# Kernel optimization log

Measured on AMD Instinct MI355X. Metric: run time of the kernel, lower is better.

## Reference

```python
import jax, jax.numpy as jnp
import numpy as np

N = 50000
E = 800000
D = 128  # in_channels == hidden_channels
NEG_SLOPE = 0.2


def setup_inputs() -> dict:
    key = jax.random.key(0)
    ks = jax.random.split(key, 20)
    x = jax.random.normal(ks[0], (N, D), dtype=jnp.float32)
    edge_index = jax.random.randint(ks[1], (2, E), 0, N, dtype=jnp.int64)
    inp = {"x": x, "edge_index": edge_index}
    # 3 GATv2 layers: lin_l (source), lin_r (target), att vector, bias. Glorot-ish scale.
    s = 1.0 / np.sqrt(D)
    for l in range(3):
        inp[f"Wl{l}"] = jax.random.normal(ks[2 + 4 * l], (D, D), dtype=jnp.float32) * s
        inp[f"Wr{l}"] = jax.random.normal(ks[3 + 4 * l], (D, D), dtype=jnp.float32) * s
        inp[f"att{l}"] = jax.random.normal(ks[4 + 4 * l], (D,), dtype=jnp.float32) * s
        inp[f"b{l}"] = jnp.zeros((D,), dtype=jnp.float32)
    return inp


def _gatv2_layer(x, src, dst, Wl, Wr, att, b):
    # PyG GATv2Conv, heads=1: xl = lin_l(x) (source side), xr = lin_r(x) (target side)
    xl = x @ Wl.T  # [N, D]
    xr = x @ Wr.T  # [N, D]
    m = xl[src] + xr[dst]                      # [E', D]
    m = jnp.where(m > 0, m, NEG_SLOPE * m)     # LeakyReLU(0.2)
    e = m @ att                                # [E'] attention logits
    # segment softmax over incoming edges of each dst node (numerically stable)
    emax = jnp.full((x.shape[0],), jnp.finfo(e.dtype).min, dtype=e.dtype).at[dst].max(e)
    ex = jnp.exp(e - emax[dst])
    denom = jnp.zeros((x.shape[0],), dtype=e.dtype).at[dst].add(ex)
    alpha = ex / denom[dst]                    # [E']
    out = jnp.zeros_like(xl).at[dst].add(alpha[:, None] * xl[src])
    return out + b


def reference(x, edge_index, Wl0, Wr0, att0, b0, Wl1, Wr1, att1, b1, Wl2, Wr2, att2, b2):
    n = x.shape[0]
    loops = jnp.arange(n, dtype=edge_index.dtype)
    src = jnp.concatenate([edge_index[0], loops])  # add_self_loops=True (PyG default)
    dst = jnp.concatenate([edge_index[1], loops])
    params = [(Wl0, Wr0, att0, b0), (Wl1, Wr1, att1, b1), (Wl2, Wr2, att2, b2)]
    h = x
    for (Wl, Wr, att, b) in params:
        h = _gatv2_layer(h, src, dst, Wl, Wr, att, b)
        h = jax.nn.gelu(h, approximate=False)  # F.gelu exact
        # dropout p=0.0 / eval mode -> identity
    return h
```

## Files before the change

kernel.cpp:

```cpp
#include <hip/hip_runtime.h>
#include <hip/hip_fp16.h>
#include <math.h>
#include <float.h>

#define NNODES 50000
#define NPAD   50048
#define NEDGES 800000
#define NETOT  (NEDGES + NNODES)
#define NBUCK  98
#define BCAP   12288
#define PCHUNK 2048

typedef __attribute__((ext_vector_type(8))) _Float16 hfrag;
typedef __attribute__((ext_vector_type(4))) float ffrag;
typedef __attribute__((ext_vector_type(8))) unsigned short ushort8;


__global__ __launch_bounds__(256) void convert_w(
    const float* __restrict__ w0, const float* __restrict__ w1,
    const float* __restrict__ w2, const float* __restrict__ w3,
    const float* __restrict__ w4, const float* __restrict__ w5,
    _Float16* __restrict__ bp)
{
  int g = blockIdx.x * 256 + threadIdx.x;
  int mat = g >> 11;
  int c = g & 2047;
  int tile_nl = c >> 8;
  int kb = (c >> 6) & 3;
  int lane = c & 63;
  int n_local = tile_nl * 16 + (lane & 15);
  int k0 = kb * 32 + (lane >> 4) * 8;
  const float* s = w0;
  if (mat == 1) s = w1; else if (mat == 2) s = w2; else if (mat == 3) s = w3;
  else if (mat == 4) s = w4; else if (mat == 5) s = w5;
  const float* src = s + n_local * 128 + k0;
  hfrag hv;
#pragma unroll
  for (int j = 0; j < 8; ++j) hv[j] = (_Float16)src[j];
  int layer = mat >> 1, half = mat & 1;
  int chunk = ((half * 8 + tile_nl) * 4 + kb) * 64 + lane;
  ((hfrag*)(bp + (size_t)layer * 32768))[chunk] = hv;
}

__global__ __launch_bounds__(256) void convert_x(
    const float* __restrict__ x, _Float16* __restrict__ ap)
{
  int g = blockIdx.x * 256 + threadIdx.x;
  if (g >= NNODES * 16) return;
  int tile_m = g >> 8;
  int kb = (g >> 6) & 3;
  int lane = g & 63;
  int m = tile_m * 16 + (lane & 15);
  int k0 = kb * 32 + (lane >> 4) * 8;
  const float4* src = (const float4*)(x + (size_t)m * 128 + k0);
  float4 v0 = src[0], v1 = src[1];
  hfrag hv;
  hv[0] = (_Float16)v0.x; hv[1] = (_Float16)v0.y;
  hv[2] = (_Float16)v0.z; hv[3] = (_Float16)v0.w;
  hv[4] = (_Float16)v1.x; hv[5] = (_Float16)v1.y;
  hv[6] = (_Float16)v1.z; hv[7] = (_Float16)v1.w;
  ((hfrag*)ap)[g] = hv;
}

__global__ __launch_bounds__(256) void partition_kernel(
    const int* __restrict__ ei, int* __restrict__ bcursor,
    unsigned* __restrict__ tmp)
{
  __shared__ unsigned stage[PCHUNK];
  __shared__ int cnt[128];
  __shared__ int lstart[NBUCK];
  __shared__ int gbase[NBUCK];
  __shared__ int lcur[NBUCK];
  const int t = threadIdx.x;
  const int e0 = blockIdx.x * PCHUNK;

  if (t < 128) cnt[t] = 0;
  __syncthreads();

  unsigned pk[8]; int pb[8]; int nv = 0;
#pragma unroll
  for (int i = 0; i < 8; ++i) {
    int e = e0 + t + i * 256;
    if (e < NETOT) {
      int s, d;
      if (e < NEDGES) { s = ei[e]; d = ei[NEDGES + e]; }
      else            { s = e - NEDGES; d = s; }
      int b = d >> 9;
      pk[nv] = (unsigned)s | ((unsigned)(d & 511) << 16) | ((unsigned)b << 25);
      pb[nv] = b;
      atomicAdd(&cnt[b], 1);
      ++nv;
    }
  }
  __syncthreads();

  int v = (t < 128) ? cnt[t] : 0;
  for (int off = 1; off < 128; off <<= 1) {
    int u = (t < 128 && t >= off) ? cnt[t - off] : 0;
    __syncthreads();
    if (t < 128) cnt[t] += u;
    __syncthreads();
  }
  if (t < NBUCK) {
    int excl = cnt[t] - v;
    lstart[t] = excl;
    lcur[t] = excl;
    gbase[t] = (v > 0) ? atomicAdd(&bcursor[t], v) : 0;
  }
  __syncthreads();

  for (int i = 0; i < nv; ++i) {
    int p = atomicAdd(&lcur[pb[i]], 1);
    stage[p] = pk[i];
  }
  __syncthreads();

  int total = cnt[NBUCK - 1];
  for (int j = t; j < total; j += 256) {
    unsigned w = stage[j];
    int b = (int)(w >> 25);
    int pos = gbase[b] + (j - lstart[b]);
    if (pos < BCAP) tmp[(size_t)b * BCAP + pos] = w;
  }
}

__global__ __launch_bounds__(256) void bucket_sort(
    const int* __restrict__ bcursor, const unsigned* __restrict__ tmp,
    int* __restrict__ rowptr, int* __restrict__ col)
{
  __shared__ int sh[512];
  __shared__ int cur[512];
  const int b = blockIdx.x;
  const int t = threadIdx.x;
  int nb = bcursor[b];
  if (nb > BCAP) nb = BCAP;

  int base = 0;
  for (int c = 0; c < b; ++c) base += bcursor[c];

  sh[t] = 0; sh[t + 256] = 0;
  __syncthreads();
  const unsigned* tb = tmp + (size_t)b * BCAP;
  for (int j = t; j < nb; j += 256)
    atomicAdd(&sh[(tb[j] >> 16) & 511], 1);
  __syncthreads();

  int c1 = sh[t], c2 = sh[t + 256];
  for (int off = 1; off < 512; off <<= 1) {
    int u1 = (t >= off) ? sh[t - off] : 0;
    int u2 = (t + 256 >= off) ? sh[t + 256 - off] : 0;
    __syncthreads();
    sh[t] += u1; sh[t + 256] += u2;
    __syncthreads();
  }
  int e1 = sh[t] - c1, e2 = sh[t + 256] - c2;
  cur[t] = e1; cur[t + 256] = e2;
  int g1 = b * 512 + t, g2 = b * 512 + t + 256;
  if (g1 < NNODES) rowptr[g1] = base + e1;
  if (g2 < NNODES) rowptr[g2] = base + e2;
  if (b == 0 && t == 0) rowptr[NNODES] = NETOT;
  __syncthreads();

  for (int j = t; j < nb; j += 256) {
    unsigned w = tb[j];
    int s = atomicAdd(&cur[(w >> 16) & 511], 1);
    col[base + s] = (int)(w & 0xFFFFu);
  }
}

__global__ __launch_bounds__(256) void gemm_mfma(
    const _Float16* __restrict__ ap, const _Float16* __restrict__ bp,
    ushort* __restrict__ xlh, float* __restrict__ xr)
{
  const int wave = threadIdx.x >> 6;
  const int lane = threadIdx.x & 63;
  const int l16  = lane & 15;
  const int kq   = lane >> 4;
  const int m0   = blockIdx.x * 32;
  const int tm0  = m0 >> 4;

  ffrag acc[2][4];
#pragma unroll
  for (int mt = 0; mt < 2; ++mt)
#pragma unroll
    for (int nt = 0; nt < 4; ++nt)
      acc[mt][nt] = (ffrag){0.f, 0.f, 0.f, 0.f};

#pragma unroll
  for (int kb = 0; kb < 4; ++kb) {
    hfrag ah[2], bh[4];
#pragma unroll
    for (int mt = 0; mt < 2; ++mt) {
      size_t o = (size_t)(((tm0 + mt) * 4 + kb) * 512 + lane * 8);
      ah[mt] = *(const hfrag*)&ap[o];
    }
#pragma unroll
    for (int nt = 0; nt < 4; ++nt) {
      size_t o = (size_t)((((wave * 4 + nt) * 4) + kb) * 512 + lane * 8);
      bh[nt] = *(const hfrag*)&bp[o];
    }
#pragma unroll
    for (int mt = 0; mt < 2; ++mt)
#pragma unroll
      for (int nt = 0; nt < 4; ++nt)
        acc[mt][nt] = __builtin_amdgcn_mfma_f32_16x16x32_f16(
            ah[mt], bh[nt], acc[mt][nt], 0, 0, 0);
  }

#pragma unroll
  for (int mt = 0; mt < 2; ++mt) {
    int mb = m0 + mt * 16 + kq * 4;
#pragma unroll
    for (int nt = 0; nt < 4; ++nt) {
      int ng = wave * 64 + nt * 16 + l16;
      if (ng < 128) {
#pragma unroll
        for (int r = 0; r < 4; ++r) {
          int m = mb + r;
          if (m < NNODES)
            ((__half*)xlh)[m * 128 + ng] = __float2half(acc[mt][nt][r]);
        }
      } else {
        int n = ng & 127;
#pragma unroll
        for (int r = 0; r < 4; ++r) {
          int m = mb + r;
          if (m < NNODES) xr[m * 128 + n] = acc[mt][nt][r];
        }
      }
    }
  }
}

static __device__ __forceinline__ void h8_to_f(
    const ushort8& v, float4& a, float4& b)
{
  a.x = __half2float(__ushort_as_half(v[0]));
  a.y = __half2float(__ushort_as_half(v[1]));
  a.z = __half2float(__ushort_as_half(v[2]));
  a.w = __half2float(__ushort_as_half(v[3]));
  b.x = __half2float(__ushort_as_half(v[4]));
  b.y = __half2float(__ushort_as_half(v[5]));
  b.z = __half2float(__ushort_as_half(v[6]));
  b.w = __half2float(__ushort_as_half(v[7]));
}

static __device__ __forceinline__ float edge_logit(
    const float4& a0, const float4& a1,
    const float4& xr0, const float4& xr1,
    const float4& t0, const float4& t1)
{
  float m, qa, qb;
  m = a0.x + xr0.x; m = fmaxf(m, 0.2f * m); qa = m * t0.x;
  m = a0.y + xr0.y; m = fmaxf(m, 0.2f * m); qa = fmaf(m, t0.y, qa);
  m = a0.z + xr0.z; m = fmaxf(m, 0.2f * m); qa = fmaf(m, t0.z, qa);
  m = a0.w + xr0.w; m = fmaxf(m, 0.2f * m); qa = fmaf(m, t0.w, qa);
  m = a1.x + xr1.x; m = fmaxf(m, 0.2f * m); qb = m * t1.x;
  m = a1.y + xr1.y; m = fmaxf(m, 0.2f * m); qb = fmaf(m, t1.y, qb);
  m = a1.z + xr1.z; m = fmaxf(m, 0.2f * m); qb = fmaf(m, t1.z, qb);
  m = a1.w + xr1.w; m = fmaxf(m, 0.2f * m); qb = fmaf(m, t1.w, qb);
  return qa + qb;
}

static __device__ __forceinline__ void facc(
    float4& a0, float4& a1, float w, const float4& v0, const float4& v1)
{
  a0.x = fmaf(w, v0.x, a0.x); a0.y = fmaf(w, v0.y, a0.y);
  a0.z = fmaf(w, v0.z, a0.z); a0.w = fmaf(w, v0.w, a0.w);
  a1.x = fmaf(w, v1.x, a1.x); a1.y = fmaf(w, v1.y, a1.y);
  a1.z = fmaf(w, v1.z, a1.z); a1.w = fmaf(w, v1.w, a1.w);
}

static __device__ __forceinline__ float gelu_exact(float v) {
  return 0.5f * v * (1.f + erff(v * 0.70710678118654752f));
}

__global__ __launch_bounds__(256) void agg_kernel(
    const int* __restrict__ rowptr, const int* __restrict__ col,
    const ushort* __restrict__ xlh, const float* __restrict__ xr,
    const float* __restrict__ att, const float* __restrict__ bias,
    float* __restrict__ hout, _Float16* __restrict__ ap, int last)
{
  const int tid = threadIdx.x;
  const int l16 = tid & 15;
  const int grp = tid >> 4;
  const int d   = blockIdx.x * 16 + grp;
  const int fb  = l16 * 2;

  const ushort8* xl8 = (const ushort8*)xlh;
  float4 xr0 = ((const float4*)xr)[d * 32 + fb];
  float4 xr1 = ((const float4*)xr)[d * 32 + fb + 1];
  float4 at0 = ((const float4*)att)[fb];
  float4 at1 = ((const float4*)att)[fb + 1];

  const int beg = rowptr[d], end = rowptr[d + 1];

  float dnE = 0.f, dnO = 0.f;
  float4 aE0 = {0,0,0,0}, aE1 = {0,0,0,0};
  float4 aO0 = {0,0,0,0}, aO1 = {0,0,0,0};

  for (int k = beg; k < end; k += 4) {
    const int  c0 = col[k];
    const bool v1 = (k + 1 < end);
    const bool v2 = (k + 2 < end);
    const bool v3 = (k + 3 < end);
    const int  c1 = col[v1 ? k + 1 : k];
    const int  c2 = col[v2 ? k + 2 : k];
    const int  c3 = col[v3 ? k + 3 : k];

    ushort8 Ar = xl8[c0 * 16 + l16];
    ushort8 Br = xl8[c1 * 16 + l16];
    ushort8 Cr = xl8[c2 * 16 + l16];
    ushort8 Dr = xl8[c3 * 16 + l16];

    float4 A0, A1, B0, B1, C0, C1, D0, D1;
    h8_to_f(Ar, A0, A1);
    h8_to_f(Br, B0, B1);
    h8_to_f(Cr, C0, C1);
    h8_to_f(Dr, D0, D1);

    float q0 = edge_logit(A0, A1, xr0, xr1, at0, at1);
    float q1 = edge_logit(B0, B1, xr0, xr1, at0, at1);
    float q2 = edge_logit(C0, C1, xr0, xr1, at0, at1);
    float q3 = edge_logit(D0, D1, xr0, xr1, at0, at1);
#pragma unroll
    for (int off = 8; off > 0; off >>= 1) {
      q0 += __shfl_xor(q0, off, 64);
      q1 += __shfl_xor(q1, off, 64);
      q2 += __shfl_xor(q2, off, 64);
      q3 += __shfl_xor(q3, off, 64);
    }
    float w0 = __expf(q0);
    float w1 = v1 ? __expf(q1) : 0.f;
    float w2 = v2 ? __expf(q2) : 0.f;
    float w3 = v3 ? __expf(q3) : 0.f;
    dnE += w0 + w2;
    dnO += w1 + w3;
    facc(aE0, aE1, w0, A0, A1);
    facc(aO0, aO1, w1, B0, B1);
    facc(aE0, aE1, w2, C0, C1);
    facc(aO0, aO1, w3, D0, D1);
  }

  const float dn = dnE + dnO;
  const float inv = 1.f / dn;
  float4 ac0, ac1;
  ac0.x = aE0.x + aO0.x; ac0.y = aE0.y + aO0.y;
  ac0.z = aE0.z + aO0.z; ac0.w = aE0.w + aO0.w;
  ac1.x = aE1.x + aO1.x; ac1.y = aE1.y + aO1.y;
  ac1.z = aE1.z + aO1.z; ac1.w = aE1.w + aO1.w;

  float4 bi0 = ((const float4*)bias)[fb];
  float4 bi1 = ((const float4*)bias)[fb + 1];
  float o0 = gelu_exact(fmaf(ac0.x, inv, bi0.x));
  float o1 = gelu_exact(fmaf(ac0.y, inv, bi0.y));
  float o2 = gelu_exact(fmaf(ac0.z, inv, bi0.z));
  float o3 = gelu_exact(fmaf(ac0.w, inv, bi0.w));
  float o4 = gelu_exact(fmaf(ac1.x, inv, bi1.x));
  float o5 = gelu_exact(fmaf(ac1.y, inv, bi1.y));
  float o6 = gelu_exact(fmaf(ac1.z, inv, bi1.z));
  float o7 = gelu_exact(fmaf(ac1.w, inv, bi1.w));

  if (last) {
    ((float4*)hout)[d * 32 + fb]     = make_float4(o0, o1, o2, o3);
    ((float4*)hout)[d * 32 + fb + 1] = make_float4(o4, o5, o6, o7);
  } else {
    hfrag hv;
    hv[0] = (_Float16)o0; hv[1] = (_Float16)o1;
    hv[2] = (_Float16)o2; hv[3] = (_Float16)o3;
    hv[4] = (_Float16)o4; hv[5] = (_Float16)o5;
    hv[6] = (_Float16)o6; hv[7] = (_Float16)o7;
    int chunk = ((d >> 4) * 4 + (l16 >> 2)) * 64 + (l16 & 3) * 16 + (d & 15);
    ((hfrag*)ap)[chunk] = hv;
  }
}

extern "C" void kernel_launch(void* const* d_in, const int* in_sizes, int n_in,
                              void* d_out, int out_size, void* d_ws, size_t ws_size,
                              hipStream_t stream)
{
  const float* x = (const float*)d_in[0];
  const int* ei = (const int*)d_in[1];
  const float *Wl[3], *Wr[3], *attv[3], *bv[3];
  for (int l = 0; l < 3; ++l) {
    Wl[l]   = (const float*)d_in[2 + 4 * l];
    Wr[l]   = (const float*)d_in[3 + 4 * l];
    attv[l] = (const float*)d_in[4 + 4 * l];
    bv[l]   = (const float*)d_in[5 + 4 * l];
  }

  char* base = (char*)d_ws;
  size_t off = 0;
  auto alloc = [&](size_t bytes) -> char* {
    char* p = base + off;
    off += (bytes + 255) & ~(size_t)255;
    return p;
  };
  _Float16* ap  = (_Float16*)alloc((size_t)NPAD * 128 * 2);
  _Float16* bp  = (_Float16*)alloc((size_t)3 * 256 * 128 * 2);
  ushort* xlh   = (ushort*)alloc((size_t)NNODES * 128 * 2);
  int* rowptr   = (int*)alloc((size_t)(NNODES + 1) * 4);
  int* col      = (int*)alloc((size_t)NETOT * 4);
  int* bcursor  = (int*)alloc((size_t)NBUCK * 4);
  unsigned* tmp = (unsigned*)alloc((size_t)NBUCK * BCAP * 4);
  float* xr     = (float*)d_out;
  (void)ws_size; (void)in_sizes; (void)n_in; (void)out_size;

  hipMemsetAsync(bcursor, 0, (size_t)NBUCK * 4, stream);
  convert_w<<<48, 256, 0, stream>>>(Wl[0], Wr[0], Wl[1], Wr[1], Wl[2], Wr[2],
                                    bp);
  convert_x<<<(NNODES * 16 + 255) / 256, 256, 0, stream>>>(x, ap);
  partition_kernel<<<(NETOT + PCHUNK - 1) / PCHUNK, 256, 0, stream>>>(
      ei, bcursor, tmp);
  bucket_sort<<<NBUCK, 256, 0, stream>>>(bcursor, tmp, rowptr, col);

  for (int l = 0; l < 3; ++l) {
    gemm_mfma<<<NPAD / 32, 256, 0, stream>>>(
        ap, bp + (size_t)l * 32768, xlh, xr);
    agg_kernel<<<NNODES / 16, 256, 0, stream>>>(
        rowptr, col, xlh, xr, attv[l], bv[l], (float*)d_out, ap,
        (l == 2) ? 1 : 0);
  }
}
```

Before: 318.4 us.

## Fuse prologue kernels, store xr in fp16, parallelize bucket base scan

Merges weight conversion, input conversion and edge partitioning into one prologue launch that branches on block index, removing two kernel launches. The target-side projection xr is now stored in fp16 in its own buffer instead of fp32 in the output buffer, halving its write and read traffic between the GEMM and aggregation kernels. The bucket sort computes its base offset with a shared-memory prefix scan instead of a serial loop per block. Storing xr in fp16 adds rounding error to the attention logits.

```diff
diff --git a/kernel.cpp b/kernel.cpp
--- a/kernel.cpp
+++ b/kernel.cpp
@@ -10,61 +10,23 @@
 #define NBUCK  98
 #define BCAP   12288
 #define PCHUNK 2048
+#define PBLK   416
+#define CWBLK  48
+#define CXBLK  3125
 
 typedef __attribute__((ext_vector_type(8))) _Float16 hfrag;
 typedef __attribute__((ext_vector_type(4))) float ffrag;
 typedef __attribute__((ext_vector_type(8))) unsigned short ushort8;
 
 
-__global__ __launch_bounds__(256) void convert_w(
+__global__ __launch_bounds__(256) void prologue_kernel(
+    const float* __restrict__ x,
     const float* __restrict__ w0, const float* __restrict__ w1,
     const float* __restrict__ w2, const float* __restrict__ w3,
     const float* __restrict__ w4, const float* __restrict__ w5,
-    _Float16* __restrict__ bp)
-{
-  int g = blockIdx.x * 256 + threadIdx.x;
-  int mat = g >> 11;
-  int c = g & 2047;
-  int tile_nl = c >> 8;
-  int kb = (c >> 6) & 3;
-  int lane = c & 63;
-  int n_local = tile_nl * 16 + (lane & 15);
-  int k0 = kb * 32 + (lane >> 4) * 8;
-  const float* s = w0;
-  if (mat == 1) s = w1; else if (mat == 2) s = w2; else if (mat == 3) s = w3;
-  else if (mat == 4) s = w4; else if (mat == 5) s = w5;
-  const float* src = s + n_local * 128 + k0;
-  hfrag hv;
-#pragma unroll
-  for (int j = 0; j < 8; ++j) hv[j] = (_Float16)src[j];
-  int layer = mat >> 1, half = mat & 1;
-  int chunk = ((half * 8 + tile_nl) * 4 + kb) * 64 + lane;
-  ((hfrag*)(bp + (size_t)layer * 32768))[chunk] = hv;
-}
-
-__global__ __launch_bounds__(256) void convert_x(
-    const float* __restrict__ x, _Float16* __restrict__ ap)
-{
-  int g = blockIdx.x * 256 + threadIdx.x;
-  if (g >= NNODES * 16) return;
-  int tile_m = g >> 8;
-  int kb = (g >> 6) & 3;
-  int lane = g & 63;
-  int m = tile_m * 16 + (lane & 15);
-  int k0 = kb * 32 + (lane >> 4) * 8;
-  const float4* src = (const float4*)(x + (size_t)m * 128 + k0);
-  float4 v0 = src[0], v1 = src[1];
-  hfrag hv;
-  hv[0] = (_Float16)v0.x; hv[1] = (_Float16)v0.y;
-  hv[2] = (_Float16)v0.z; hv[3] = (_Float16)v0.w;
-  hv[4] = (_Float16)v1.x; hv[5] = (_Float16)v1.y;
-  hv[6] = (_Float16)v1.z; hv[7] = (_Float16)v1.w;
-  ((hfrag*)ap)[g] = hv;
-}
-
-__global__ __launch_bounds__(256) void partition_kernel(
-    const int* __restrict__ ei, int* __restrict__ bcursor,
-    unsigned* __restrict__ tmp)
+    const int* __restrict__ ei,
+    _Float16* __restrict__ ap, _Float16* __restrict__ bp,
+    int* __restrict__ bcursor, unsigned* __restrict__ tmp)
 {
   __shared__ unsigned stage[PCHUNK];
   __shared__ int cnt[128];
@@ -72,55 +34,94 @@
   __shared__ int gbase[NBUCK];
   __shared__ int lcur[NBUCK];
   const int t = threadIdx.x;
-  const int e0 = blockIdx.x * PCHUNK;
-
-  if (t < 128) cnt[t] = 0;
-  __syncthreads();
-
-  unsigned pk[8]; int pb[8]; int nv = 0;
-#pragma unroll
-  for (int i = 0; i < 8; ++i) {
-    int e = e0 + t + i * 256;
-    if (e < NETOT) {
-      int s, d;
-      if (e < NEDGES) { s = ei[e]; d = ei[NEDGES + e]; }
-      else            { s = e - NEDGES; d = s; }
-      int b = d >> 9;
-      pk[nv] = (unsigned)s | ((unsigned)(d & 511) << 16) | ((unsigned)b << 25);
-      pb[nv] = b;
-      atomicAdd(&cnt[b], 1);
-      ++nv;
-    }
-  }
-  __syncthreads();
-
-  int v = (t < 128) ? cnt[t] : 0;
-  for (int off = 1; off < 128; off <<= 1) {
-    int u = (t < 128 && t >= off) ? cnt[t - off] : 0;
-    __syncthreads();
-    if (t < 128) cnt[t] += u;
-    __syncthreads();
-  }
-  if (t < NBUCK) {
-    int excl = cnt[t] - v;
-    lstart[t] = excl;
-    lcur[t] = excl;
-    gbase[t] = (v > 0) ? atomicAdd(&bcursor[t], v) : 0;
-  }
-  __syncthreads();
-
-  for (int i = 0; i < nv; ++i) {
-    int p = atomicAdd(&lcur[pb[i]], 1);
-    stage[p] = pk[i];
-  }
-  __syncthreads();
-
-  int total = cnt[NBUCK - 1];
-  for (int j = t; j < total; j += 256) {
-    unsigned w = stage[j];
-    int b = (int)(w >> 25);
-    int pos = gbase[b] + (j - lstart[b]);
-    if (pos < BCAP) tmp[(size_t)b * BCAP + pos] = w;
+  const int blk = blockIdx.x;
+
+  if (blk < PBLK) {
+    const int e0 = blk * PCHUNK;
+    if (t < 128) cnt[t] = 0;
+    __syncthreads();
+
+    unsigned pk[8]; int pb[8]; int nv = 0;
+#pragma unroll
+    for (int i = 0; i < 8; ++i) {
+      int e = e0 + t + i * 256;
+      if (e < NETOT) {
+        int s, d;
+        if (e < NEDGES) { s = ei[e]; d = ei[NEDGES + e]; }
+        else            { s = e - NEDGES; d = s; }
+        int b = d >> 9;
+        pk[nv] = (unsigned)s | ((unsigned)(d & 511) << 16) |
+                 ((unsigned)b << 25);
+        pb[nv] = b;
+        atomicAdd(&cnt[b], 1);
+        ++nv;
+      }
+    }
+    __syncthreads();
+
+    int v = (t < 128) ? cnt[t] : 0;
+    for (int off = 1; off < 128; off <<= 1) {
+      int u = (t < 128 && t >= off) ? cnt[t - off] : 0;
+      __syncthreads();
+      if (t < 128) cnt[t] += u;
+      __syncthreads();
+    }
+    if (t < NBUCK) {
+      int excl = cnt[t] - v;
+      lstart[t] = excl;
+      lcur[t] = excl;
+      gbase[t] = (v > 0) ? atomicAdd(&bcursor[t], v) : 0;
+    }
+    __syncthreads();
+
+    for (int i = 0; i < nv; ++i) {
+      int p = atomicAdd(&lcur[pb[i]], 1);
+      stage[p] = pk[i];
+    }
+    __syncthreads();
+
+    int total = cnt[NBUCK - 1];
+    for (int j = t; j < total; j += 256) {
+      unsigned w = stage[j];
+      int b = (int)(w >> 25);
+      int pos = gbase[b] + (j - lstart[b]);
+      if (pos < BCAP) tmp[(size_t)b * BCAP + pos] = w;
+    }
+  } else if (blk < PBLK + CWBLK) {
+    int g = (blk - PBLK) * 256 + t;
+    int mat = g >> 11;
+    int c = g & 2047;
+    int tile_nl = c >> 8;
+    int kb = (c >> 6) & 3;
+    int lane = c & 63;
+    int n_local = tile_nl * 16 + (lane & 15);
+    int k0 = kb * 32 + (lane >> 4) * 8;
+    const float* s = w0;
+    if (mat == 1) s = w1; else if (mat == 2) s = w2;
+    else if (mat == 3) s = w3; else if (mat == 4) s = w4;
+    else if (mat == 5) s = w5;
+    const float* src = s + n_local * 128 + k0;
+    hfrag hv;
+#pragma unroll
+    for (int j = 0; j < 8; ++j) hv[j] = (_Float16)src[j];
+    int layer = mat >> 1, half = mat & 1;
+    int chunk = ((half * 8 + tile_nl) * 4 + kb) * 64 + lane;
+    ((hfrag*)(bp + (size_t)layer * 32768))[chunk] = hv;
+  } else {
+    int g = (blk - PBLK - CWBLK) * 256 + t;
+    int tile_m = g >> 8;
+    int kb = (g >> 6) & 3;
+    int lane = g & 63;
+    int m = tile_m * 16 + (lane & 15);
+    int k0 = kb * 32 + (lane >> 4) * 8;
+    const float4* src = (const float4*)(x + (size_t)m * 128 + k0);
+    float4 v0 = src[0], v1 = src[1];
+    hfrag hv;
+    hv[0] = (_Float16)v0.x; hv[1] = (_Float16)v0.y;
+    hv[2] = (_Float16)v0.z; hv[3] = (_Float16)v0.w;
+    hv[4] = (_Float16)v1.x; hv[5] = (_Float16)v1.y;
+    hv[6] = (_Float16)v1.z; hv[7] = (_Float16)v1.w;
+    ((hfrag*)ap)[g] = hv;
   }
 }
 
@@ -132,11 +133,20 @@
   __shared__ int cur[512];
   const int b = blockIdx.x;
   const int t = threadIdx.x;
-  int nb = bcursor[b];
+
+  int bc = (t < NBUCK) ? bcursor[t] : 0;
+  if (t < 128) sh[t] = bc;
+  __syncthreads();
+  for (int off = 1; off < 128; off <<= 1) {
+    int u = (t < 128 && t >= off) ? sh[t - off] : 0;
+    __syncthreads();
+    if (t < 128) sh[t] += u;
+    __syncthreads();
+  }
+  const int base = (b > 0) ? sh[b - 1] : 0;
+  int nb = sh[b] - base;
   if (nb > BCAP) nb = BCAP;
-
-  int base = 0;
-  for (int c = 0; c < b; ++c) base += bcursor[c];
+  __syncthreads();
 
   sh[t] = 0; sh[t + 256] = 0;
   __syncthreads();
@@ -170,7 +180,7 @@
 
 __global__ __launch_bounds__(256) void gemm_mfma(
     const _Float16* __restrict__ ap, const _Float16* __restrict__ bp,
-    ushort* __restrict__ xlh, float* __restrict__ xr)
+    _Float16* __restrict__ xlh, _Float16* __restrict__ xrh)
 {
   const int wave = threadIdx.x >> 6;
   const int lane = threadIdx.x & 63;
@@ -217,15 +227,14 @@
 #pragma unroll
         for (int r = 0; r < 4; ++r) {
           int m = mb + r;
-          if (m < NNODES)
-            ((__half*)xlh)[m * 128 + ng] = __float2half(acc[mt][nt][r]);
+          if (m < NNODES) xlh[m * 128 + ng] = (_Float16)acc[mt][nt][r];
         }
       } else {
         int n = ng & 127;
 #pragma unroll
         for (int r = 0; r < 4; ++r) {
           int m = mb + r;
-          if (m < NNODES) xr[m * 128 + n] = acc[mt][nt][r];
+          if (m < NNODES) xrh[m * 128 + n] = (_Float16)acc[mt][nt][r];
         }
       }
     }
@@ -277,7 +286,7 @@
 
 __global__ __launch_bounds__(256) void agg_kernel(
     const int* __restrict__ rowptr, const int* __restrict__ col,
-    const ushort* __restrict__ xlh, const float* __restrict__ xr,
+    const ushort* __restrict__ xlh, const ushort* __restrict__ xrh,
     const float* __restrict__ att, const float* __restrict__ bias,
     float* __restrict__ hout, _Float16* __restrict__ ap, int last)
 {
@@ -288,8 +297,9 @@
   const int fb  = l16 * 2;
 
   const ushort8* xl8 = (const ushort8*)xlh;
-  float4 xr0 = ((const float4*)xr)[d * 32 + fb];
-  float4 xr1 = ((const float4*)xr)[d * 32 + fb + 1];
+  ushort8 xrr = ((const ushort8*)xrh)[d * 16 + l16];
+  float4 xr0, xr1;
+  h8_to_f(xrr, xr0, xr1);
   float4 at0 = ((const float4*)att)[fb];
   float4 at1 = ((const float4*)att)[fb + 1];
 
@@ -398,27 +408,24 @@
   };
   _Float16* ap  = (_Float16*)alloc((size_t)NPAD * 128 * 2);
   _Float16* bp  = (_Float16*)alloc((size_t)3 * 256 * 128 * 2);
-  ushort* xlh   = (ushort*)alloc((size_t)NNODES * 128 * 2);
+  _Float16* xlh = (_Float16*)alloc((size_t)NNODES * 128 * 2);
+  _Float16* xrh = (_Float16*)alloc((size_t)NNODES * 128 * 2);
   int* rowptr   = (int*)alloc((size_t)(NNODES + 1) * 4);
   int* col      = (int*)alloc((size_t)NETOT * 4);
   int* bcursor  = (int*)alloc((size_t)NBUCK * 4);
   unsigned* tmp = (unsigned*)alloc((size_t)NBUCK * BCAP * 4);
-  float* xr     = (float*)d_out;
   (void)ws_size; (void)in_sizes; (void)n_in; (void)out_size;
 
   hipMemsetAsync(bcursor, 0, (size_t)NBUCK * 4, stream);
-  convert_w<<<48, 256, 0, stream>>>(Wl[0], Wr[0], Wl[1], Wr[1], Wl[2], Wr[2],
-                                    bp);
-  convert_x<<<(NNODES * 16 + 255) / 256, 256, 0, stream>>>(x, ap);
-  partition_kernel<<<(NETOT + PCHUNK - 1) / PCHUNK, 256, 0, stream>>>(
-      ei, bcursor, tmp);
+  prologue_kernel<<<PBLK + CWBLK + CXBLK, 256, 0, stream>>>(
+      x, Wl[0], Wr[0], Wl[1], Wr[1], Wl[2], Wr[2], ei, ap, bp, bcursor, tmp);
   bucket_sort<<<NBUCK, 256, 0, stream>>>(bcursor, tmp, rowptr, col);
 
   for (int l = 0; l < 3; ++l) {
     gemm_mfma<<<NPAD / 32, 256, 0, stream>>>(
-        ap, bp + (size_t)l * 32768, xlh, xr);
+        ap, bp + (size_t)l * 32768, xlh, xrh);
     agg_kernel<<<NNODES / 16, 256, 0, stream>>>(
-        rowptr, col, xlh, xr, attv[l], bv[l], (float*)d_out, ap,
-        (l == 2) ? 1 : 0);
-  }
-}
+        rowptr, col, (const ushort*)xlh, (const ushort*)xrh, attv[l], bv[l],
+        (float*)d_out, ap, (l == 2) ? 1 : 0);
+  }
+}
```

New measurement: 307.9 us. -3.3%, faster.
